# Kernel optimization log

Measured on AMD Instinct MI355X. Metric: run time of the kernel, lower is better.

## Reference

```python
import jax, jax.numpy as jnp
import numpy as np

N = 5000        # nodes
F = 7699        # node feature dim (fixed by code)
E = 40000       # edges
ED = 3          # edge_dim (fixed by code)
H1, C1 = 4, 1024
H2, C2 = 1, 1024
NUM_OUT = 128
NEG_SLOPE = 0.2


def _glorot(key, shape):
    fan_in = shape[0]
    return jax.random.normal(key, shape, jnp.float32) / np.float32(np.sqrt(fan_in))


def setup_inputs() -> dict:
    key = jax.random.key(0)
    ks = jax.random.split(key, 16)
    x = jax.random.normal(ks[0], (N, F), jnp.float32)
    src = jax.random.randint(ks[1], (E,), 0, N)
    dst = jax.random.randint(ks[2], (E,), 0, N)
    src = jnp.where(src == dst, (src + 1) % N, src)  # no pre-existing self loops
    edge_index = jnp.stack([src, dst]).astype(jnp.int32)
    edge_attr = jax.random.normal(ks[3], (E, ED), jnp.float32)
    inp = {
        "x": x, "edge_index": edge_index, "edge_attr": edge_attr,
        # GATv2Conv #1: 7699 -> 1024, heads=4, edge_dim=3
        "W1l": _glorot(ks[4], (F, H1 * C1)), "b1l": jnp.zeros((H1 * C1,), jnp.float32),
        "W1r": _glorot(ks[5], (F, H1 * C1)), "b1r": jnp.zeros((H1 * C1,), jnp.float32),
        "W1e": _glorot(ks[6], (ED, H1 * C1)),
        "att1": _glorot(ks[7], (H1, C1)),
        "bias1": jnp.zeros((H1 * C1,), jnp.float32),
        # GATv2Conv #2: 4096 -> 1024, heads=1, edge_dim=3
        "W2l": _glorot(ks[8], (H1 * C1, H2 * C2)), "b2l": jnp.zeros((H2 * C2,), jnp.float32),
        "W2r": _glorot(ks[9], (H1 * C1, H2 * C2)), "b2r": jnp.zeros((H2 * C2,), jnp.float32),
        "W2e": _glorot(ks[10], (ED, H2 * C2)),
        "att2": _glorot(ks[11], (H2, C2)),
        "bias2": jnp.zeros((H2 * C2,), jnp.float32),
        # final Linear(1024, num_outputs)
        "Wlin": _glorot(ks[12], (C2, NUM_OUT)), "blin": jnp.zeros((NUM_OUT,), jnp.float32),
    }
    return inp


def gatv2_layer(x, src, dst, edge_attr, Wl, bl, Wr, br, We, att, bias, heads, out_ch):
    """PyG GATv2Conv with add_self_loops=True, fill_value='mean', concat=True."""
    n = x.shape[0]
    # self-loop edge_attr = mean of incoming edge attrs per node (fill_value='mean')
    deg = jax.ops.segment_sum(jnp.ones((src.shape[0],), jnp.float32), dst, num_segments=n)
    loop_attr = jax.ops.segment_sum(edge_attr, dst, num_segments=n) / jnp.maximum(deg, 1.0)[:, None]
    idx = jnp.arange(n, dtype=src.dtype)
    srcf = jnp.concatenate([src, idx])
    dstf = jnp.concatenate([dst, idx])
    ea = jnp.concatenate([edge_attr, loop_attr], axis=0)
    xl = (x @ Wl + bl).reshape(n, heads, out_ch)   # lin_l (source)
    xr = (x @ Wr + br).reshape(n, heads, out_ch)   # lin_r (target)
    ee = (ea @ We).reshape(-1, heads, out_ch)       # lin_edge (no bias)
    e = jax.nn.leaky_relu(xl[srcf] + xr[dstf] + ee, NEG_SLOPE)  # [E', H, C]
    logit = jnp.einsum('ehc,hc->eh', e, att)                     # [E', H]
    # segment softmax over destination nodes (every node has a self loop)
    m = jax.lax.stop_gradient(jax.ops.segment_max(logit, dstf, num_segments=n))
    a = jnp.exp(logit - m[dstf])
    denom = jax.ops.segment_sum(a, dstf, num_segments=n)
    alpha = a / (denom[dstf] + 1e-16)
    out = jax.ops.segment_sum(alpha[:, :, None] * xl[srcf], dstf, num_segments=n)  # [N,H,C]
    return out.reshape(n, heads * out_ch) + bias


def reference(x, edge_index, edge_attr,
              W1l, b1l, W1r, b1r, W1e, att1, bias1,
              W2l, b2l, W2r, b2r, W2e, att2, bias2,
              Wlin, blin):
    src, dst = edge_index[0], edge_index[1]
    h = gatv2_layer(x, src, dst, edge_attr, W1l, b1l, W1r, b1r, W1e, att1, bias1, H1, C1)
    h = gatv2_layer(h, src, dst, edge_attr, W2l, b2l, W2r, b2r, W2e, att2, bias2, H2, C2)
    return h @ Wlin + blin
```

## Files before the change

### kernel.cpp

```cpp
#include <hip/hip_runtime.h>
#include <cstdint>
#include <cstddef>

#define N_NODES 5000
#define F_IN    7699
#define KP1     7712
#define KT1     241
#define MP      5120
#define E_EDGES 40000
#define EFULL   45000
#define HC1     4096
#define N1      8192
#define HC2     1024
#define N2      2048
#define NOUT    128
#define GM256   (MP / 256)
#define GM128   (MP / 128)

typedef __bf16 bf16x8 __attribute__((ext_vector_type(8)));
typedef float  f32x4  __attribute__((ext_vector_type(4)));
typedef float  f32x16 __attribute__((ext_vector_type(16)));
typedef unsigned short u16x8 __attribute__((ext_vector_type(8)));
typedef _Float16 f16;
typedef _Float16 f16x8 __attribute__((ext_vector_type(8)));

using as1_uchar = unsigned char __attribute__((address_space(1)));
using as3_uchar = unsigned char __attribute__((address_space(3)));

__device__ __forceinline__ unsigned short f2bf(float f) {
  union { float f; unsigned int u; } v; v.f = f;
  return (unsigned short)((v.u + 0x7fffu + ((v.u >> 16) & 1u)) >> 16);
}
__device__ __forceinline__ float bf2f(unsigned short h) {
  union { unsigned int u; float f; } v; v.u = ((unsigned int)h) << 16;
  return v.f;
}

__device__ __forceinline__ void gload16(const void* g, void* l) {
  __builtin_amdgcn_global_load_lds(
      reinterpret_cast<const as1_uchar*>(reinterpret_cast<uintptr_t>(g)),
      reinterpret_cast<as3_uchar*>(reinterpret_cast<uintptr_t>(l)),
      16, 0, 0);
}



__global__ void k_split_x(const float* __restrict__ x, unsigned short* __restrict__ hi,
                          unsigned short* __restrict__ lo) {
  const int C8 = KP1 / 8;
  int ci = blockIdx.x * 256 + threadIdx.x;
  if (ci >= MP * C8) return;
  int r = ci / C8, c8 = ci % C8;
  int c = c8 * 8;
  u16x8 hb, lb;
  #pragma unroll
  for (int j = 0; j < 8; ++j) {
    float v = 0.f;
    if (r < N_NODES && (c + j) < F_IN) v = x[(size_t)r * F_IN + c + j];
    unsigned short h = f2bf(v);
    hb[j] = h; lb[j] = f2bf(v - bf2f(h));
  }
  size_t off = ((size_t)((r >> 7) * KT1 + (c >> 5)) * 4 + ((c >> 3) & 3)) * 1024 + (r & 127) * 8;
  *(u16x8*)&hi[off] = hb;
  *(u16x8*)&lo[off] = lb;
}


__global__ void k_split_w(const float* __restrict__ W,
                          unsigned short* __restrict__ hi, unsigned short* __restrict__ lo,
                          int K, int Nsrc, int c0, int KT, int rowOffset) {
  __shared__ float tile[32][33];
  const int tid = threadIdx.x;
  const int kt = blockIdx.x;
  const int n0 = blockIdx.y * 32;
  #pragma unroll
  for (int i = tid >> 5; i < 32; i += 8) {
    int k = kt * 32 + i;
    tile[i][tid & 31] = (k < K) ? W[(size_t)k * Nsrc + c0 + n0 + (tid & 31)] : 0.f;
  }
  __syncthreads();
  if (tid < 128) {
    const int nn = tid >> 2, kc = (tid & 3) << 3;
    const int n = rowOffset + n0 + nn;
    u16x8 hb, lb;
    #pragma unroll
    for (int j = 0; j < 8; ++j) {
      float v = tile[kc + j][nn];
      unsigned short h = f2bf(v);
      hb[j] = h; lb[j] = f2bf(v - bf2f(h));
    }
    size_t off = ((size_t)((n >> 7) * KT + kt) * 4 + (kc >> 3)) * 1024 + (n & 127) * 8;
    *(u16x8*)&hi[off] = hb;
    *(u16x8*)&lo[off] = lb;
  }
}


template <int OF16>
__global__ __launch_bounds__(512, 2) void k_gemm_big(
    const unsigned short* __restrict__ Ahi, const unsigned short* __restrict__ Alo,
    const unsigned short* __restrict__ Bhi, const unsigned short* __restrict__ Blo,
    void* __restrict__ Cp, const float* __restrict__ bias0, const float* __restrict__ bias1,
    int halfN, int M, int Nc, int ldC, int KT32, int nbn)
{
  __shared__ __align__(16) unsigned short S[4 * 12288];

  const int tid = threadIdx.x;
  const int lane = tid & 63;
  const int w = tid >> 6;
  const int wm = w >> 1, wn = w & 1;

  const int nwg = gridDim.x;
  const int qq = nwg >> 3, rr = nwg & 7;
  const int xcd = blockIdx.x & 7, idx = blockIdx.x >> 3;
  const int wg = (xcd < rr ? xcd * (qq + 1) : rr * (qq + 1) + (xcd - rr) * qq) + idx;
  const int bm = wg / nbn, bn = wg % nbn;

  f32x16 acc[2][2] = {};

  const unsigned short* gsrc[3];
  int dd[3];
  #pragma unroll
  for (int s = 0; s < 3; ++s) {
    const int q = w * 3 + s;
    const unsigned short* base; int dOff; size_t rowoff; int p, hf;
    if (q < 8)       { int r_ = q;      base = Ahi; int t = r_ >> 2; p = (r_ >> 1) & 1; hf = r_ & 1;
                       dOff = t * 2048 + p * 1024 + hf * 512; rowoff = (size_t)(bm * 2 + t) * KT32 * 4096; }
    else if (q < 16) { int r_ = q - 8;  base = Alo; int t = r_ >> 2; p = (r_ >> 1) & 1; hf = r_ & 1;
                       dOff = 4096 + t * 2048 + p * 1024 + hf * 512; rowoff = (size_t)(bm * 2 + t) * KT32 * 4096; }
    else if (q < 20) { int r_ = q - 16; base = Bhi; p = (r_ >> 1) & 1; hf = r_ & 1;
                       dOff = 8192 + p * 1024 + hf * 512; rowoff = (size_t)bn * KT32 * 4096; }
    else             { int r_ = q - 20; base = Blo; p = (r_ >> 1) & 1; hf = r_ & 1;
                       dOff = 10240 + p * 1024 + hf * 512; rowoff = (size_t)bn * KT32 * 4096; }
    gsrc[s] = base + rowoff + p * 1024 + hf * 512 + lane * 8;
    dd[s] = dOff;
  }

  auto stage = [&](int kt16, int bufo) {
    const size_t o = (size_t)kt16 * 2048;
    #pragma unroll
    for (int s = 0; s < 3; ++s) gload16(gsrc[s] + o, &S[bufo + dd[s]]);
  };

  const int r5 = lane & 31, h5 = lane >> 5;
  const int tA = wm >> 1;
  const int rrA = (wm & 1) * 64;
  int ra[2], cb[2];
  #pragma unroll
  for (int i = 0; i < 2; ++i) ra[i] = tA * 2048 + h5 * 1024 + (rrA + i * 32 + r5) * 8;
  #pragma unroll
  for (int j = 0; j < 2; ++j) cb[j] = 8192 + h5 * 1024 + (wn * 64 + j * 32 + r5) * 8;

  struct Frags { bf16x8 ah[2], al[2], bh[2], bl[2]; };
  auto rdfr = [&](Frags& f, int bufo) {
    #pragma unroll
    for (int i = 0; i < 2; ++i) {
      f.ah[i] = *(const bf16x8*)&S[bufo + ra[i]];
      f.al[i] = *(const bf16x8*)&S[bufo + 4096 + ra[i]];
    }
    #pragma unroll
    for (int j = 0; j < 2; ++j) {
      f.bh[j] = *(const bf16x8*)&S[bufo + cb[j]];
      f.bl[j] = *(const bf16x8*)&S[bufo + 2048 + cb[j]];
    }
  };
  auto domfma = [&](Frags& f) {
    __builtin_amdgcn_s_setprio(1);
    #pragma unroll
    for (int j = 0; j < 2; ++j)
      #pragma unroll
      for (int i = 0; i < 2; ++i) {
        acc[i][j] = __builtin_amdgcn_mfma_f32_32x32x16_bf16(f.ah[i], f.bh[j], acc[i][j], 0, 0, 0);
        acc[i][j] = __builtin_amdgcn_mfma_f32_32x32x16_bf16(f.al[i], f.bh[j], acc[i][j], 0, 0, 0);
        acc[i][j] = __builtin_amdgcn_mfma_f32_32x32x16_bf16(f.ah[i], f.bl[j], acc[i][j], 0, 0, 0);
      }
    __builtin_amdgcn_s_setprio(0);
  };

  const int KT16 = KT32 * 2;

  stage(0, 0);
  stage(1, 12288);
  stage(2, 24576);
  asm volatile("s_waitcnt vmcnt(3)" ::: "memory");
  __builtin_amdgcn_s_barrier();
  Frags fA, fB;
  rdfr(fA, 0);

  int o0 = 0, o1 = 12288, o2 = 24576, o3 = 36864;
  for (int kt = 0; kt < KT16; kt += 2) {
    stage((kt + 3 < KT16) ? kt + 3 : KT16 - 1, o3);
    rdfr(fB, o1);
    domfma(fA);
    asm volatile("s_waitcnt vmcnt(3)" ::: "memory");
    __builtin_amdgcn_s_barrier();
    stage((kt + 4 < KT16) ? kt + 4 : KT16 - 1, o0);
    rdfr(fA, o2);
    domfma(fB);
    asm volatile("s_waitcnt vmcnt(3)" ::: "memory");
    __builtin_amdgcn_s_barrier();
    int t0 = o0, t1 = o1;
    o0 = o2; o1 = o3; o2 = t0; o3 = t1;
  }

  #pragma unroll
  for (int i = 0; i < 2; ++i) {
    #pragma unroll
    for (int j = 0; j < 2; ++j) {
      const int gc = bn * 128 + wn * 64 + j * 32 + r5;
      if (gc < Nc) {
        const float bv = (gc < halfN) ? bias0[gc] : bias1[gc - halfN];
        #pragma unroll
        for (int reg = 0; reg < 16; ++reg) {
          const int gr = bm * 256 + wm * 64 + i * 32 + (reg & 3) + 8 * (reg >> 2) + 4 * h5;
          if (gr < M) {
            float v = acc[i][j][reg] + bv;
            if (OF16) ((f16*)Cp)[(size_t)gr * ldC + gc] = (f16)v;
            else      ((float*)Cp)[(size_t)gr * ldC + gc] = v;
          }
        }
      }
    }
  }
}


template <int OF16>
__global__ __launch_bounds__(256, 2) void k_gemm_bb(
    const unsigned short* __restrict__ Ahi, const unsigned short* __restrict__ Alo,
    const unsigned short* __restrict__ Bhi, const unsigned short* __restrict__ Blo,
    void* __restrict__ Cp, const float* __restrict__ bias0, const float* __restrict__ bias1,
    int halfN, int M, int Nc, int ldC, int KT32, int nbn)
{
  __shared__ __align__(16) unsigned short S[4 * 8192];

  const int tid = threadIdx.x;
  const int lane = tid & 63;
  const int w = tid >> 6;
  const int wm = w >> 1, wn = w & 1;

  const int nwg = gridDim.x;
  const int qq = nwg >> 3, rr = nwg & 7;
  const int xcd = blockIdx.x & 7, idx = blockIdx.x >> 3;
  const int wg = (xcd < rr ? xcd * (qq + 1) : rr * (qq + 1) + (xcd - rr) * qq) + idx;
  const int bm = wg / nbn, bn = wg % nbn;

  f32x16 acc[2][2] = {};

  const unsigned short* gbase = (w == 0) ? Ahi : (w == 1) ? Alo : (w == 2) ? Bhi : Blo;
  const int brow = (w < 2) ? bm : bn;
  const unsigned short* gsrc[4];
  int dd[4];
  #pragma unroll
  for (int s = 0; s < 4; ++s) {
    const int p = s >> 1, hf = s & 1;
    gsrc[s] = gbase + (size_t)brow * KT32 * 4096 + p * 1024 + hf * 512 + lane * 8;
    dd[s] = w * 2048 + p * 1024 + hf * 512;
  }

  auto stage = [&](int kt16, int bufo) {
    const size_t o = (size_t)kt16 * 2048;
    #pragma unroll
    for (int s = 0; s < 4; ++s) gload16(gsrc[s] + o, &S[bufo + dd[s]]);
  };

  const int r5 = lane & 31, h5 = lane >> 5;
  int ra[2], cb[2];
  #pragma unroll
  for (int i = 0; i < 2; ++i) ra[i] = h5 * 1024 + (wm * 64 + i * 32 + r5) * 8;
  #pragma unroll
  for (int j = 0; j < 2; ++j) cb[j] = 4096 + h5 * 1024 + (wn * 64 + j * 32 + r5) * 8;

  struct Frags { bf16x8 ah[2], al[2], bh[2], bl[2]; };
  auto rdfr = [&](Frags& f, int bufo) {
    #pragma unroll
    for (int i = 0; i < 2; ++i) {
      f.ah[i] = *(const bf16x8*)&S[bufo + ra[i]];
      f.al[i] = *(const bf16x8*)&S[bufo + 2048 + ra[i]];
    }
    #pragma unroll
    for (int j = 0; j < 2; ++j) {
      f.bh[j] = *(const bf16x8*)&S[bufo + cb[j]];
      f.bl[j] = *(const bf16x8*)&S[bufo + 2048 + cb[j]];
    }
  };
  auto domfma = [&](Frags& f) {
    __builtin_amdgcn_s_setprio(1);
    #pragma unroll
    for (int j = 0; j < 2; ++j)
      #pragma unroll
      for (int i = 0; i < 2; ++i) {
        acc[i][j] = __builtin_amdgcn_mfma_f32_32x32x16_bf16(f.ah[i], f.bh[j], acc[i][j], 0, 0, 0);
        acc[i][j] = __builtin_amdgcn_mfma_f32_32x32x16_bf16(f.al[i], f.bh[j], acc[i][j], 0, 0, 0);
        acc[i][j] = __builtin_amdgcn_mfma_f32_32x32x16_bf16(f.ah[i], f.bl[j], acc[i][j], 0, 0, 0);
      }
    __builtin_amdgcn_s_setprio(0);
  };

  const int KT16 = KT32 * 2;

  stage(0, 0);
  stage(1, 8192);
  stage(2, 16384);
  asm volatile("s_waitcnt vmcnt(4)" ::: "memory");
  __builtin_amdgcn_s_barrier();
  Frags fA, fB;
  rdfr(fA, 0);

  int o0 = 0, o1 = 8192, o2 = 16384, o3 = 24576;
  for (int kt = 0; kt < KT16; kt += 2) {
    stage((kt + 3 < KT16) ? kt + 3 : KT16 - 1, o3);
    rdfr(fB, o1);
    domfma(fA);
    asm volatile("s_waitcnt vmcnt(4)" ::: "memory");
    __builtin_amdgcn_s_barrier();
    stage((kt + 4 < KT16) ? kt + 4 : KT16 - 1, o0);
    rdfr(fA, o2);
    domfma(fB);
    asm volatile("s_waitcnt vmcnt(4)" ::: "memory");
    __builtin_amdgcn_s_barrier();
    int t0 = o0, t1 = o1;
    o0 = o2; o1 = o3; o2 = t0; o3 = t1;
  }

  #pragma unroll
  for (int i = 0; i < 2; ++i) {
    #pragma unroll
    for (int j = 0; j < 2; ++j) {
      const int gc = bn * 128 + wn * 64 + j * 32 + r5;
      if (gc < Nc) {
        const float bv = (gc < halfN) ? bias0[gc] : bias1[gc - halfN];
        #pragma unroll
        for (int reg = 0; reg < 16; ++reg) {
          const int gr = bm * 128 + wm * 64 + i * 32 + (reg & 3) + 8 * (reg >> 2) + 4 * h5;
          if (gr < M) {
            float v = acc[i][j][reg] + bv;
            if (OF16) ((f16*)Cp)[(size_t)gr * ldC + gc] = (f16)v;
            else      ((float*)Cp)[(size_t)gr * ldC + gc] = v;
          }
        }
      }
    }
  }
}


__global__ void k_deg(const int* __restrict__ dst, const float* __restrict__ ea,
                      float* __restrict__ deg, float* __restrict__ lattr, int E) {
  int e = blockIdx.x * 256 + threadIdx.x;
  if (e >= E) return;
  int d = dst[e];
  atomicAdd(&deg[d], 1.f);
  atomicAdd(&lattr[d * 3 + 0], ea[e * 3 + 0]);
  atomicAdd(&lattr[d * 3 + 1], ea[e * 3 + 1]);
  atomicAdd(&lattr[d * 3 + 2], ea[e * 3 + 2]);
}

__global__ void k_lattr_fin(float* __restrict__ lattr, const float* __restrict__ deg, int n) {
  int i = blockIdx.x * 256 + threadIdx.x;
  if (i >= n) return;
  float dv = fmaxf(deg[i], 1.f);
  lattr[i * 3 + 0] /= dv; lattr[i * 3 + 1] /= dv; lattr[i * 3 + 2] /= dv;
}

__global__ void k_eafull(const float* __restrict__ ea, const float* __restrict__ lattr,
                         float* __restrict__ eaf, int E, int n) {
  int e = blockIdx.x * 256 + threadIdx.x;
  if (e >= E + n) return;
  const float* s = (e < E) ? &ea[(size_t)e * 3] : &lattr[(size_t)(e - E) * 3];
  eaf[e * 3 + 0] = s[0]; eaf[e * 3 + 1] = s[1]; eaf[e * 3 + 2] = s[2];
}

__global__ void k_count(const int* __restrict__ dst, int* __restrict__ cnt, int E, int n) {
  int e = blockIdx.x * 256 + threadIdx.x;
  if (e >= E + n) return;
  int d = (e < E) ? dst[e] : (e - E);
  atomicAdd(&cnt[d], 1);
}

__global__ void k_scan(const int* __restrict__ cnt, int* __restrict__ rowptr, int n) {
  int lane = threadIdx.x;
  int run = 0;
  for (int base = 0; base < n; base += 64) {
    int i = base + lane;
    int v = (i < n) ? cnt[i] : 0;
    #pragma unroll
    for (int off = 1; off < 64; off <<= 1) {
      int t = __shfl_up(v, off, 64);
      if (lane >= off) v += t;
    }
    if (i < n) rowptr[i + 1] = run + v;
    run += __shfl(v, 63, 64);
  }
  if (lane == 0) rowptr[0] = 0;
}

__global__ void k_fill(const int* __restrict__ dst, const int* __restrict__ rowptr,
                       int* __restrict__ fillc, int* __restrict__ elist, int E, int n) {
  int e = blockIdx.x * 256 + threadIdx.x;
  if (e >= E + n) return;
  int d = (e < E) ? dst[e] : (e - E);
  int pos = rowptr[d] + atomicAdd(&fillc[d], 1);
  elist[pos] = e;
}


template <int H, int ITERS>
__global__ __launch_bounds__(256) void k_attn(
    const f16* __restrict__ xl, const f16* __restrict__ xr, int strideX,
    const float* __restrict__ eaf, const float* __restrict__ We, const float* __restrict__ att,
    const int* __restrict__ rowptr, const int* __restrict__ elist, const int* __restrict__ src,
    int E, const float* __restrict__ bias,
    unsigned short* __restrict__ ohi, unsigned short* __restrict__ olo, int KTo)
{
  constexpr int HC = ITERS * 256;
  const int n = blockIdx.x;
  const int tid = threadIdx.x;
  __shared__ float red[H][4];
  __shared__ float wbr[H], rbr[H], dsh[H];
  __shared__ float sx[HC];

  float xrv[ITERS], w0[ITERS], w1[ITERS], w2[ITERS], av[ITERS];
  const f16* rr = xr + (size_t)n * strideX;
  #pragma unroll
  for (int i = 0; i < ITERS; ++i) {
    const int hc = tid + (i << 8);
    xrv[i] = (float)rr[hc];
    w0[i] = We[hc]; w1[i] = We[HC + hc]; w2[i] = We[2 * HC + hc];
    av[i] = att[hc];
  }
  float acc[ITERS];
  #pragma unroll
  for (int i = 0; i < ITERS; ++i) acc[i] = 0.f;
  float mh = -1e30f, sh = 0.f;
  const int lane = tid & 63, wv = tid >> 6;
  const int start = rowptr[n], end = rowptr[n + 1];

  for (int p = start; p < end; ++p) {
    const int e = elist[p];
    const int s = (e < E) ? src[e] : (e - E);
    const float ea0 = eaf[e * 3 + 0], ea1 = eaf[e * 3 + 1], ea2 = eaf[e * 3 + 2];
    const f16* rl = xl + (size_t)s * strideX;
    float xlv[ITERS];
    float accL[H];
    #pragma unroll
    for (int h = 0; h < H; ++h) accL[h] = 0.f;
    #pragma unroll
    for (int i = 0; i < ITERS; ++i) {
      const int hc = tid + (i << 8);
      xlv[i] = (float)rl[hc];
      float v = xlv[i] + xrv[i] + ea0 * w0[i] + ea1 * w1[i] + ea2 * w2[i];
      v = (v > 0.f) ? v : 0.2f * v;
      accL[i >> 2] += v * av[i];
    }
    #pragma unroll
    for (int h = 0; h < H; ++h) {
      float v = accL[h];
      #pragma unroll
      for (int off = 32; off > 0; off >>= 1) v += __shfl_down(v, off, 64);
      if (lane == 0) red[h][wv] = v;
    }
    __syncthreads();
    if (tid < H) {
      const float l = red[tid][0] + red[tid][1] + red[tid][2] + red[tid][3];
      const float mn = fmaxf(mh, l);
      const float r_ = __expf(mh - mn), w_ = __expf(l - mn);
      sh = sh * r_ + w_;
      mh = mn;
      wbr[tid] = w_; rbr[tid] = r_;
    }
    __syncthreads();
    #pragma unroll
    for (int i = 0; i < ITERS; ++i) {
      const int h = (H == 4) ? (i >> 2) : 0;
      acc[i] = acc[i] * rbr[h] + wbr[h] * xlv[i];
    }
  }

  if (tid < H) dsh[tid] = sh + 1e-16f;
  __syncthreads();
  #pragma unroll
  for (int i = 0; i < ITERS; ++i) {
    const int hc = tid + (i << 8);
    const int h = (H == 4) ? (i >> 2) : 0;
    sx[hc] = acc[i] / dsh[h] + bias[hc];
  }
  __syncthreads();

  constexpr int NC8 = (HC / 8 + 255) / 256;
  #pragma unroll
  for (int q = 0; q < NC8; ++q) {
    const int c8 = tid + q * 256;
    if (c8 * 8 < HC) {
      u16x8 hb, lb;
      #pragma unroll
      for (int j = 0; j < 8; ++j) {
        float v = sx[c8 * 8 + j];
        unsigned short h = f2bf(v);
        hb[j] = h; lb[j] = f2bf(v - bf2f(h));
      }
      size_t off = ((size_t)((n >> 7) * KTo + (c8 >> 2)) * 4 + (c8 & 3)) * 1024 + (n & 127) * 8;
      *(u16x8*)&ohi[off] = hb;
      *(u16x8*)&olo[off] = lb;
    }
  }
}


extern "C" void kernel_launch(void* const* d_in, const int* in_sizes, int n_in,
                              void* d_out, int out_size, void* d_ws, size_t ws_size,
                              hipStream_t stream) {
  const float* x    = (const float*)d_in[0];
  const int*   eidx = (const int*)d_in[1];
  const float* eattr= (const float*)d_in[2];
  const float* W1l  = (const float*)d_in[3];
  const float* b1l  = (const float*)d_in[4];
  const float* W1r  = (const float*)d_in[5];
  const float* b1r  = (const float*)d_in[6];
  const float* W1e  = (const float*)d_in[7];
  const float* att1 = (const float*)d_in[8];
  const float* bias1= (const float*)d_in[9];
  const float* W2l  = (const float*)d_in[10];
  const float* b2l  = (const float*)d_in[11];
  const float* W2r  = (const float*)d_in[12];
  const float* b2r  = (const float*)d_in[13];
  const float* W2e  = (const float*)d_in[14];
  const float* att2 = (const float*)d_in[15];
  const float* bias2= (const float*)d_in[16];
  const float* Wlin = (const float*)d_in[17];
  const float* blin = (const float*)d_in[18];
  float* out = (float*)d_out;

  char* ws = (char*)d_ws;
  const int* srcp = eidx;
  const int* dstp = eidx + E_EDGES;

  auto alignup = [](size_t v) { return (v + 255) & ~(size_t)255; };

  size_t mo = 0;
  auto take = [&](size_t sz) { size_t r = mo; mo = alignup(mo + sz); return r; };
  const size_t oLATTR = take((size_t)N_NODES * 3 * 4);
  const size_t oDEG   = take((size_t)N_NODES * 4);
  const size_t oEAF   = take((size_t)EFULL * 3 * 4);
  const size_t oCNT   = take((size_t)N_NODES * 4);
  const size_t oROW   = take((size_t)(N_NODES + 1) * 4);
  const size_t oFILL  = take((size_t)N_NODES * 4);
  const size_t oELIST = take((size_t)EFULL * 4);
  const size_t oLOGIT = take((size_t)EFULL * 4 * 4);
  const size_t oMB    = take((size_t)N_NODES * 4 * 4);
  const size_t oDB    = take((size_t)N_NODES * 4 * 4);
  const size_t oXHI   = take((size_t)MP * KP1 * 2);
  const size_t oXLO   = take((size_t)MP * KP1 * 2);
  const size_t oXLR   = take((size_t)N_NODES * N1 * 2);
  const size_t oBH    = take((size_t)N1 * KP1 * 2);
  const size_t oBL    = take((size_t)N1 * KP1 * 2);
  if (ws_size < mo) return;

  const size_t oH1HI = oXHI;
  const size_t oH1LO = oXLO;
  const size_t oXLR2 = oXLR;
  const size_t oH2HI = oXLR + 32ull * 1024 * 1024;
  const size_t oH2LO = oXLR + 48ull * 1024 * 1024;
  const size_t oB2H  = oBH;
  const size_t oB2L  = oBH + 32ull * 1024 * 1024;
  const size_t oB3H  = oBH;
  const size_t oB3L  = oBH + 1ull * 1024 * 1024;

  unsigned short* XHI  = (unsigned short*)(ws + oXHI);
  unsigned short* XLO  = (unsigned short*)(ws + oXLO);
  f16*            XLR  = (f16*)(ws + oXLR);
  unsigned short* BH   = (unsigned short*)(ws + oBH);
  unsigned short* BL   = (unsigned short*)(ws + oBL);
  float*          LATTR= (float*)(ws + oLATTR);
  float*          DEG  = (float*)(ws + oDEG);
  float*          EAF  = (float*)(ws + oEAF);
  int*            CNT  = (int*)(ws + oCNT);
  int*            ROWP = (int*)(ws + oROW);
  int*            FILLC= (int*)(ws + oFILL);
  int*            ELIST= (int*)(ws + oELIST);
  unsigned short* H1HI = (unsigned short*)(ws + oH1HI);
  unsigned short* H1LO = (unsigned short*)(ws + oH1LO);
  f16*            XLR2 = (f16*)(ws + oXLR2);
  unsigned short* H2HI = (unsigned short*)(ws + oH2HI);
  unsigned short* H2LO = (unsigned short*)(ws + oH2LO);
  unsigned short* B2H  = (unsigned short*)(ws + oB2H);
  unsigned short* B2L  = (unsigned short*)(ws + oB2L);
  unsigned short* B3H  = (unsigned short*)(ws + oB3H);
  unsigned short* B3L  = (unsigned short*)(ws + oB3L);
  (void)oLOGIT; (void)oMB; (void)oDB;

  hipMemsetAsync(ws + oDEG,   0, (size_t)N_NODES * 4, stream);
  hipMemsetAsync(ws + oLATTR, 0, (size_t)N_NODES * 3 * 4, stream);
  hipMemsetAsync(ws + oCNT,   0, (size_t)N_NODES * 4, stream);
  hipMemsetAsync(ws + oFILL,  0, (size_t)N_NODES * 4, stream);

  const int gE  = (E_EDGES + 255) / 256;
  const int gEF = (EFULL + 255) / 256;
  const int gN  = (N_NODES + 255) / 256;

  k_deg<<<gE, 256, 0, stream>>>(dstp, eattr, DEG, LATTR, E_EDGES);
  k_lattr_fin<<<gN, 256, 0, stream>>>(LATTR, DEG, N_NODES);
  k_eafull<<<gEF, 256, 0, stream>>>(eattr, LATTR, EAF, E_EDGES, N_NODES);
  k_count<<<gEF, 256, 0, stream>>>(dstp, CNT, E_EDGES, N_NODES);
  k_scan<<<1, 64, 0, stream>>>(CNT, ROWP, N_NODES);
  k_fill<<<gEF, 256, 0, stream>>>(dstp, ROWP, FILLC, ELIST, E_EDGES, N_NODES);

  k_split_x<<<MP * (KP1 / 8) / 256, 256, 0, stream>>>(x, XHI, XLO);
  k_split_w<<<dim3(KT1, HC1 / 32), 256, 0, stream>>>(W1l, BH, BL, F_IN, HC1, 0, KT1, 0);
  k_split_w<<<dim3(KT1, HC1 / 32), 256, 0, stream>>>(W1r, BH, BL, F_IN, HC1, 0, KT1, HC1);
  k_gemm_big<1><<<GM256 * (N1 / 128), 512, 0, stream>>>(
      XHI, XLO, BH, BL, XLR, b1l, b1r, HC1, N_NODES, N1, N1, KT1, N1 / 128);

  hipMemsetAsync(ws + oH1HI, 0, (size_t)MP * HC1 * 2, stream);
  hipMemsetAsync(ws + oH1LO, 0, (size_t)MP * HC1 * 2, stream);
  k_attn<4, 16><<<N_NODES, 256, 0, stream>>>(
      XLR, XLR + HC1, N1, EAF, W1e, att1, ROWP, ELIST, srcp, E_EDGES,
      bias1, H1HI, H1LO, HC1 / 32);

  k_split_w<<<dim3(HC1 / 32, HC2 / 32), 256, 0, stream>>>(W2l, B2H, B2L, HC1, HC2, 0, HC1 / 32, 0);
  k_split_w<<<dim3(HC1 / 32, HC2 / 32), 256, 0, stream>>>(W2r, B2H, B2L, HC1, HC2, 0, HC1 / 32, HC2);
  k_gemm_bb<1><<<GM128 * (N2 / 128), 256, 0, stream>>>(
      H1HI, H1LO, B2H, B2L, XLR2, b2l, b2r, HC2, N_NODES, N2, N2, HC1 / 32, N2 / 128);

  hipMemsetAsync(ws + oH2HI, 0, (size_t)MP * HC2 * 2, stream);
  hipMemsetAsync(ws + oH2LO, 0, (size_t)MP * HC2 * 2, stream);
  k_attn<1, 4><<<N_NODES, 256, 0, stream>>>(
      XLR2, XLR2 + HC2, N2, EAF, W2e, att2, ROWP, ELIST, srcp, E_EDGES,
      bias2, H2HI, H2LO, HC2 / 32);

  k_split_w<<<dim3(HC2 / 32, NOUT / 32), 256, 0, stream>>>(Wlin, B3H, B3L, HC2, NOUT, 0, HC2 / 32, 0);
  k_gemm_bb<0><<<GM128 * 1, 256, 0, stream>>>(
      H2HI, H2LO, B3H, B3L, out, blin, blin, NOUT, N_NODES, NOUT, NOUT, HC2 / 32, 1);
}
```

Baseline: 2.588 ms.

## Map each attention head to one wavefront and pack nodes per block

The attention kernel is restructured so each thread owns 16 contiguous channels, which makes one 64-lane wavefront cover exactly one head. The per-head logit then comes from a wave shuffle reduction, and the two block-wide barriers per edge plus the shared-memory staging are gone. The xl and xr gathers become vectorised 16-byte f16 loads. Layer 2, which has 1024 channels, now packs four nodes per 256-thread block, one node per wave. The trade-off is that each thread now holds more registers.

```diff
diff --git a/kernel.cpp b/kernel.cpp
--- a/kernel.cpp
+++ b/kernel.cpp
@@ -405,104 +405,78 @@
 }
 
 
-template <int H, int ITERS>
+template <int HC, int NPB>
 __global__ __launch_bounds__(256) void k_attn(
     const f16* __restrict__ xl, const f16* __restrict__ xr, int strideX,
     const float* __restrict__ eaf, const float* __restrict__ We, const float* __restrict__ att,
     const int* __restrict__ rowptr, const int* __restrict__ elist, const int* __restrict__ src,
     int E, const float* __restrict__ bias,
-    unsigned short* __restrict__ ohi, unsigned short* __restrict__ olo, int KTo)
+    unsigned short* __restrict__ ohi, unsigned short* __restrict__ olo)
 {
-  constexpr int HC = ITERS * 256;
-  const int n = blockIdx.x;
-  const int tid = threadIdx.x;
-  __shared__ float red[H][4];
-  __shared__ float wbr[H], rbr[H], dsh[H];
-  __shared__ float sx[HC];
-
-  float xrv[ITERS], w0[ITERS], w1[ITERS], w2[ITERS], av[ITERS];
-  const f16* rr = xr + (size_t)n * strideX;
-  #pragma unroll
-  for (int i = 0; i < ITERS; ++i) {
-    const int hc = tid + (i << 8);
-    xrv[i] = (float)rr[hc];
-    w0[i] = We[hc]; w1[i] = We[HC + hc]; w2[i] = We[2 * HC + hc];
-    av[i] = att[hc];
-  }
-  float acc[ITERS];
-  #pragma unroll
-  for (int i = 0; i < ITERS; ++i) acc[i] = 0.f;
+  constexpr int KTo = HC / 32;
+  const int tl = (NPB == 1) ? (int)threadIdx.x : (int)(threadIdx.x & 63);
+  const int n  = blockIdx.x * NPB + ((NPB == 1) ? 0 : (int)(threadIdx.x >> 6));
+  const int base = tl * 16;
+
+  float xrv[16], w0[16], w1[16], w2[16], av[16];
+  {
+    const f16* rr = xr + (size_t)n * strideX + base;
+    f16x8 a0 = *(const f16x8*)rr, a1 = *(const f16x8*)(rr + 8);
+    #pragma unroll
+    for (int j = 0; j < 8; ++j) { xrv[j] = (float)a0[j]; xrv[8 + j] = (float)a1[j]; }
+  }
+  #pragma unroll
+  for (int j = 0; j < 16; ++j) {
+    w0[j] = We[base + j]; w1[j] = We[HC + base + j]; w2[j] = We[2 * HC + base + j];
+    av[j] = att[base + j];
+  }
+  float acc[16];
+  #pragma unroll
+  for (int j = 0; j < 16; ++j) acc[j] = 0.f;
   float mh = -1e30f, sh = 0.f;
-  const int lane = tid & 63, wv = tid >> 6;
+
   const int start = rowptr[n], end = rowptr[n + 1];
-
   for (int p = start; p < end; ++p) {
     const int e = elist[p];
     const int s = (e < E) ? src[e] : (e - E);
     const float ea0 = eaf[e * 3 + 0], ea1 = eaf[e * 3 + 1], ea2 = eaf[e * 3 + 2];
-    const f16* rl = xl + (size_t)s * strideX;
-    float xlv[ITERS];
-    float accL[H];
-    #pragma unroll
-    for (int h = 0; h < H; ++h) accL[h] = 0.f;
-    #pragma unroll
-    for (int i = 0; i < ITERS; ++i) {
-      const int hc = tid + (i << 8);
-      xlv[i] = (float)rl[hc];
-      float v = xlv[i] + xrv[i] + ea0 * w0[i] + ea1 * w1[i] + ea2 * w2[i];
+    const f16* rl = xl + (size_t)s * strideX + base;
+    f16x8 a0 = *(const f16x8*)rl, a1 = *(const f16x8*)(rl + 8);
+    float xlv[16];
+    #pragma unroll
+    for (int j = 0; j < 8; ++j) { xlv[j] = (float)a0[j]; xlv[8 + j] = (float)a1[j]; }
+    float part = 0.f;
+    #pragma unroll
+    for (int j = 0; j < 16; ++j) {
+      float v = xlv[j] + xrv[j] + ea0 * w0[j] + ea1 * w1[j] + ea2 * w2[j];
       v = (v > 0.f) ? v : 0.2f * v;
-      accL[i >> 2] += v * av[i];
-    }
-    #pragma unroll
-    for (int h = 0; h < H; ++h) {
-      float v = accL[h];
-      #pragma unroll
-      for (int off = 32; off > 0; off >>= 1) v += __shfl_down(v, off, 64);
-      if (lane == 0) red[h][wv] = v;
-    }
-    __syncthreads();
-    if (tid < H) {
-      const float l = red[tid][0] + red[tid][1] + red[tid][2] + red[tid][3];
-      const float mn = fmaxf(mh, l);
-      const float r_ = __expf(mh - mn), w_ = __expf(l - mn);
-      sh = sh * r_ + w_;
-      mh = mn;
-      wbr[tid] = w_; rbr[tid] = r_;
-    }
-    __syncthreads();
-    #pragma unroll
-    for (int i = 0; i < ITERS; ++i) {
-      const int h = (H == 4) ? (i >> 2) : 0;
-      acc[i] = acc[i] * rbr[h] + wbr[h] * xlv[i];
-    }
-  }
-
-  if (tid < H) dsh[tid] = sh + 1e-16f;
-  __syncthreads();
-  #pragma unroll
-  for (int i = 0; i < ITERS; ++i) {
-    const int hc = tid + (i << 8);
-    const int h = (H == 4) ? (i >> 2) : 0;
-    sx[hc] = acc[i] / dsh[h] + bias[hc];
-  }
-  __syncthreads();
-
-  constexpr int NC8 = (HC / 8 + 255) / 256;
-  #pragma unroll
-  for (int q = 0; q < NC8; ++q) {
-    const int c8 = tid + q * 256;
-    if (c8 * 8 < HC) {
-      u16x8 hb, lb;
-      #pragma unroll
-      for (int j = 0; j < 8; ++j) {
-        float v = sx[c8 * 8 + j];
-        unsigned short h = f2bf(v);
-        hb[j] = h; lb[j] = f2bf(v - bf2f(h));
-      }
-      size_t off = ((size_t)((n >> 7) * KTo + (c8 >> 2)) * 4 + (c8 & 3)) * 1024 + (n & 127) * 8;
-      *(u16x8*)&ohi[off] = hb;
-      *(u16x8*)&olo[off] = lb;
-    }
+      part += v * av[j];
+    }
+    #pragma unroll
+    for (int off = 32; off > 0; off >>= 1) part += __shfl_down(part, off, 64);
+    const float l = __shfl(part, 0, 64);
+    const float mn = fmaxf(mh, l);
+    const float r_ = __expf(mh - mn), w_ = __expf(l - mn);
+    sh = sh * r_ + w_;
+    mh = mn;
+    #pragma unroll
+    for (int j = 0; j < 16; ++j) acc[j] = acc[j] * r_ + w_ * xlv[j];
+  }
+
+  const float inv = 1.f / (sh + 1e-16f);
+  #pragma unroll
+  for (int q = 0; q < 2; ++q) {
+    u16x8 hb, lb;
+    #pragma unroll
+    for (int j = 0; j < 8; ++j) {
+      float v = acc[q * 8 + j] * inv + bias[base + q * 8 + j];
+      unsigned short h = f2bf(v);
+      hb[j] = h; lb[j] = f2bf(v - bf2f(h));
+    }
+    const int c8 = 2 * tl + q;
+    size_t off = ((size_t)((n >> 7) * KTo + (c8 >> 2)) * 4 + (c8 & 3)) * 1024 + (n & 127) * 8;
+    *(u16x8*)&ohi[off] = hb;
+    *(u16x8*)&olo[off] = lb;
   }
 }
 
@@ -613,9 +587,9 @@
 
   hipMemsetAsync(ws + oH1HI, 0, (size_t)MP * HC1 * 2, stream);
   hipMemsetAsync(ws + oH1LO, 0, (size_t)MP * HC1 * 2, stream);
-  k_attn<4, 16><<<N_NODES, 256, 0, stream>>>(
+  k_attn<HC1, 1><<<N_NODES, 256, 0, stream>>>(
       XLR, XLR + HC1, N1, EAF, W1e, att1, ROWP, ELIST, srcp, E_EDGES,
-      bias1, H1HI, H1LO, HC1 / 32);
+      bias1, H1HI, H1LO);
 
   k_split_w<<<dim3(HC1 / 32, HC2 / 32), 256, 0, stream>>>(W2l, B2H, B2L, HC1, HC2, 0, HC1 / 32, 0);
   k_split_w<<<dim3(HC1 / 32, HC2 / 32), 256, 0, stream>>>(W2r, B2H, B2L, HC1, HC2, 0, HC1 / 32, HC2);
@@ -624,9 +598,9 @@
 
   hipMemsetAsync(ws + oH2HI, 0, (size_t)MP * HC2 * 2, stream);
   hipMemsetAsync(ws + oH2LO, 0, (size_t)MP * HC2 * 2, stream);
-  k_attn<1, 4><<<N_NODES, 256, 0, stream>>>(
+  k_attn<HC2, 4><<<(N_NODES + 3) / 4, 256, 0, stream>>>(
       XLR2, XLR2 + HC2, N2, EAF, W2e, att2, ROWP, ELIST, srcp, E_EDGES,
-      bias2, H2HI, H2LO, HC2 / 32);
+      bias2, H2HI, H2LO);
 
   k_split_w<<<dim3(HC2 / 32, NOUT / 32), 256, 0, stream>>>(Wlin, B3H, B3L, HC2, NOUT, 0, HC2 / 32, 0);
   k_gemm_bb<0><<<GM128 * 1, 256, 0, stream>>>(
```

After: 2.543 ms. About the same (-1.8%).
